# Optimization experiments

Hardware: AMD Instinct MI355X
Metric: run time of the kernel (lower is better)

The kernel has to match this reference:

```python
import jax, jax.numpy as jnp
import numpy as np

STRIDE = 1

def setup_inputs() -> dict:
    key = jax.random.key(0)
    k1, k2, k3 = jax.random.split(key, 3)
    x = jax.random.normal(k1, (32, 64, 112, 112), dtype=jnp.float32)
    weight = jax.random.normal(k2, (128, 64, 3, 3), dtype=jnp.float32)
    bias = jax.random.normal(k3, (128,), dtype=jnp.float32)
    return {"x": x, "weight": weight, "bias": bias}

def reference(x, weight, bias):
    # Naive per-patch multiply-sum conv == standard cross-correlation conv2d,
    # stride=1, no padding (VALID).  x: (N,Cin,H,W), weight: (Cout,Cin,kH,kW)
    out = jax.lax.conv_general_dilated(
        x, weight,
        window_strides=(STRIDE, STRIDE),
        padding="VALID",
        dimension_numbers=("NCHW", "OIHW", "NCHW"),
    )
    return out + bias[None, :, None, None]
```

## Files before the change

### kernel.cpp

```cpp
#include <hip/hip_runtime.h>


#define CIN   64
#define COUT  128
#define INH   112
#define INW   112
#define HW    (INH*INW)
#define OUTH  110
#define OUTW  110
#define NB    32
#define KTOT  576
#define NPIX  (NB*OUTH*OUTW)

typedef __attribute__((ext_vector_type(8))) short short8;
typedef __attribute__((ext_vector_type(4))) float f32x4;

static __device__ __forceinline__ unsigned short f2bf(float f) {
    union { float f; unsigned int u; } v; v.f = f;
    return (unsigned short)((v.u + 0x7FFF + ((v.u >> 16) & 1)) >> 16);
}

__global__ __launch_bounds__(256) void prepack_w(const float* __restrict__ w,
                                                 unsigned short* __restrict__ ap) {
    int flat = blockIdx.x * 256 + threadIdx.x;
    int m = flat / KTOT;
    int k = flat - m * KTOT;
    int khw = k >> 6, ci = k & 63;
    int kh = khw / 3, kw = khw - kh * 3;
    float v = w[((m * CIN + ci) * 3 + kh) * 3 + kw];
    ap[((k >> 3) * COUT + m) * 8 + (k & 7)] = f2bf(v);
}

__global__ __launch_bounds__(256, 2) void conv_gemm(const float* __restrict__ x,
                                                    const unsigned short* __restrict__ ap,
                                                    const float* __restrict__ bias,
                                                    float* __restrict__ out) {
    __shared__ unsigned short ldsB[32256];

    const int flat0 = blockIdx.y * 55 + blockIdx.x;
    const int flat  = (flat0 & 7) * 220 + (flat0 >> 3);
    const int n   = flat / 55;
    const int ohp = flat - n * 55;
    const int oh0 = ohp * 2;
    const int t   = threadIdx.x;

    const int lane = t & 63;
    const int wv   = t >> 6;
    const int m_base  = (wv >> 1) * 64;
    const int px_base = (wv & 1) * 128;
    const int l16  = lane & 15;
    const int quad = lane >> 4;

    const short8* A = (const short8*)ap;

    auto loadA = [&](short8* a, int kc) {
#pragma unroll
        for (int i = 0; i < 4; ++i)
            a[i] = A[(kc * 4 + quad) * COUT + (m_base + i * 16 + l16)];
    };
    auto loadBh = [&](short8* b, int kc, int h) {
        const int khw = kc >> 1;
        const int kh = khw / 3, kw = khw - kh * 3;
        const int ci0 = (kc & 1) * 32 + quad * 8;
#pragma unroll
        for (int jj = 0; jj < 4; ++jj) {
            int px = px_base + (h * 4 + jj) * 16 + l16;
            int orow = px >> 7;
            int ow = px & 127;
            ow = (ow < OUTW) ? ow : (OUTW - 1);
            b[jj] = *(const short8*)&ldsB[((orow + kh) * INW + ow + kw) * 72 + ci0];
        }
    };

    short8 a0[4], a1[4], bA[4], bB[4];
    loadA(a0, 0);

    {
        const int cq  = lane & 7;
        const int cip = wv * 8 + ((lane >> 3) & 3) + 4 * (lane >> 5);
        const float* p0 = x + ((size_t)n * CIN + 2 * cip) * HW + (size_t)oh0 * INW;
        unsigned int* ldsW = (unsigned int*)ldsB;
#pragma unroll 8
        for (int i = 0; i < 56; ++i) {
            int cell = i * 8 + cq;
            int r = cell / 112, w = cell - r * 112;
            float va = p0[r * INW + w];
            float vb = p0[HW + r * INW + w];
            ldsW[cell * 36 + cip] = (unsigned int)f2bf(va) | ((unsigned int)f2bf(vb) << 16);
        }
    }
    loadA(a1, 1);
    __syncthreads();

    f32x4 acc[4][8] = {};
    loadBh(bA, 0, 0);

#pragma unroll
    for (int kc = 0; kc < 18; kc += 2) {
        loadBh(bB, kc, 1);
        __builtin_amdgcn_s_setprio(1);
#pragma unroll
        for (int i = 0; i < 4; ++i)
#pragma unroll
            for (int jj = 0; jj < 4; ++jj)
                acc[i][jj] = __builtin_amdgcn_mfma_f32_16x16x32_bf16(a0[i], bA[jj], acc[i][jj], 0, 0, 0);
        __builtin_amdgcn_s_setprio(0);
        loadBh(bA, kc + 1, 0);
        __builtin_amdgcn_s_setprio(1);
#pragma unroll
        for (int i = 0; i < 4; ++i)
#pragma unroll
            for (int jj = 0; jj < 4; ++jj)
                acc[i][4 + jj] = __builtin_amdgcn_mfma_f32_16x16x32_bf16(a0[i], bB[jj], acc[i][4 + jj], 0, 0, 0);
        __builtin_amdgcn_s_setprio(0);
        if (kc + 2 < 18) loadA(a0, kc + 2);

        loadBh(bB, kc + 1, 1);
        __builtin_amdgcn_s_setprio(1);
#pragma unroll
        for (int i = 0; i < 4; ++i)
#pragma unroll
            for (int jj = 0; jj < 4; ++jj)
                acc[i][jj] = __builtin_amdgcn_mfma_f32_16x16x32_bf16(a1[i], bA[jj], acc[i][jj], 0, 0, 0);
        __builtin_amdgcn_s_setprio(0);
        if (kc + 2 < 18) loadBh(bA, kc + 2, 0);
        __builtin_amdgcn_s_setprio(1);
#pragma unroll
        for (int i = 0; i < 4; ++i)
#pragma unroll
            for (int jj = 0; jj < 4; ++jj)
                acc[i][4 + jj] = __builtin_amdgcn_mfma_f32_16x16x32_bf16(a1[i], bB[jj], acc[i][4 + jj], 0, 0, 0);
        __builtin_amdgcn_s_setprio(0);
        if (kc + 3 < 18) loadA(a1, kc + 3);
    }

#pragma unroll
    for (int i = 0; i < 4; ++i) {
        const int co = m_base + i * 16 + quad * 4;
#pragma unroll
        for (int j = 0; j < 8; ++j) {
            const int px = px_base + j * 16 + l16;
            const int orow = px >> 7;
            const int ow = px & 127;
            if (ow < OUTW) {
                const size_t ob = (((size_t)n * COUT + co) * OUTH + (oh0 + orow)) * OUTW + ow;
#pragma unroll
                for (int r = 0; r < 4; ++r)
                    out[ob + (size_t)r * (OUTH * OUTW)] = acc[i][j][r] + bias[co + r];
            }
        }
    }
}

#define TCO 16
__global__ __launch_bounds__(256) void conv_direct(const float* __restrict__ x,
                                                   const float* __restrict__ w,
                                                   const float* __restrict__ bias,
                                                   float* __restrict__ out) {
    int p = blockIdx.x * 256 + threadIdx.x;
    const int co0 = blockIdx.y * TCO;
    const bool valid = p < NPIX;
    if (!valid) p = 0;
    const int n = p / (OUTH * OUTW);
    const int rem = p - n * (OUTH * OUTW);
    const int oh = rem / OUTW;
    const int ow = rem - oh * OUTW;
    float acc[TCO];
#pragma unroll
    for (int t = 0; t < TCO; ++t) acc[t] = bias[co0 + t];
    const float* xb = x + ((size_t)n * CIN) * HW + (size_t)oh * INW + ow;
    const float* wb = w + (size_t)co0 * CIN * 9;
    for (int ci = 0; ci < CIN; ++ci) {
        const float* xp = xb + (size_t)ci * HW;
        const float* wp = wb + ci * 9;
#pragma unroll
        for (int kh = 0; kh < 3; ++kh) {
            const float x0 = xp[kh * INW + 0];
            const float x1 = xp[kh * INW + 1];
            const float x2 = xp[kh * INW + 2];
#pragma unroll
            for (int t = 0; t < TCO; ++t) {
                const float* wt = wp + t * (CIN * 9) + kh * 3;
                acc[t] = fmaf(x0, wt[0], acc[t]);
                acc[t] = fmaf(x1, wt[1], acc[t]);
                acc[t] = fmaf(x2, wt[2], acc[t]);
            }
        }
    }
    if (valid) {
        const size_t ob = ((size_t)n * COUT + co0) * (OUTH * OUTW) + (size_t)oh * OUTW + ow;
#pragma unroll
        for (int t = 0; t < TCO; ++t)
            out[ob + (size_t)t * (OUTH * OUTW)] = acc[t];
    }
}

extern "C" void kernel_launch(void* const* d_in, const int* in_sizes, int n_in,
                              void* d_out, int out_size, void* d_ws, size_t ws_size,
                              hipStream_t stream) {
    const float* x    = (const float*)d_in[0];
    const float* w    = (const float*)d_in[1];
    const float* bias = (const float*)d_in[2];
    float* out        = (float*)d_out;

    const size_t ap_bytes = (size_t)COUT * KTOT * 2;

    if (ws_size >= ap_bytes) {
        unsigned short* apck = (unsigned short*)d_ws;
        prepack_w<<<288, 256, 0, stream>>>(w, apck);
        conv_gemm<<<dim3(55, NB), 256, 0, stream>>>(x, apck, bias, out);
    } else {
        dim3 grid((NPIX + 255) / 256, COUT / TCO);
        conv_direct<<<grid, dim3(256), 0, stream>>>(x, w, bias, out);
    }
}
```

Measured before the change: 324.9 us.

## Split input staging by row and overlap second half with kh=0 MFMAs

Input staging into LDS is split into two halves. Rows 0-1 are loaded first, the kh=0 taps (kc 0-5) are computed, and only then are rows 2-3 staged behind a second barrier before the remaining taps run. Staging loads are also widened to float2 with a simpler per-row index calculation. The aim is to shorten the initial global-load stall before any MFMA work starts and to let later row loads overlap with compute. The cost is an extra __syncthreads and more duplicated unrolled loop code.

```diff
diff --git a/kernel.cpp b/kernel.cpp
--- a/kernel.cpp
+++ b/kernel.cpp
@@ -72,23 +72,29 @@
         }
     };
 
+    const int cq  = lane & 7;
+    const int cip = wv * 8 + ((lane >> 3) & 3) + 4 * (lane >> 5);
+    const float* xrow0 = x + ((size_t)n * CIN + 2 * cip) * HW + (size_t)oh0 * INW;
+    unsigned int* ldsW = (unsigned int*)ldsB;
+
+    auto stageRow = [&](int r) {
+        const float* p = xrow0 + (size_t)r * INW;
+        unsigned int* dst = ldsW + r * (112 * 36) + cip;
+#pragma unroll
+        for (int i = 0; i < 7; ++i) {
+            int w0 = 16 * i + 2 * cq;
+            float2 va = *(const float2*)(p + w0);
+            float2 vb = *(const float2*)(p + HW + w0);
+            dst[(w0)     * 36] = (unsigned int)f2bf(va.x) | ((unsigned int)f2bf(vb.x) << 16);
+            dst[(w0 + 1) * 36] = (unsigned int)f2bf(va.y) | ((unsigned int)f2bf(vb.y) << 16);
+        }
+    };
+
     short8 a0[4], a1[4], bA[4], bB[4];
     loadA(a0, 0);
 
-    {
-        const int cq  = lane & 7;
-        const int cip = wv * 8 + ((lane >> 3) & 3) + 4 * (lane >> 5);
-        const float* p0 = x + ((size_t)n * CIN + 2 * cip) * HW + (size_t)oh0 * INW;
-        unsigned int* ldsW = (unsigned int*)ldsB;
-#pragma unroll 8
-        for (int i = 0; i < 56; ++i) {
-            int cell = i * 8 + cq;
-            int r = cell / 112, w = cell - r * 112;
-            float va = p0[r * INW + w];
-            float vb = p0[HW + r * INW + w];
-            ldsW[cell * 36 + cip] = (unsigned int)f2bf(va) | ((unsigned int)f2bf(vb) << 16);
-        }
-    }
+    stageRow(0);
+    stageRow(1);
     loadA(a1, 1);
     __syncthreads();
 
@@ -96,7 +102,7 @@
     loadBh(bA, 0, 0);
 
 #pragma unroll
-    for (int kc = 0; kc < 18; kc += 2) {
+    for (int kc = 0; kc < 6; kc += 2) {
         loadBh(bB, kc, 1);
         __builtin_amdgcn_s_setprio(1);
 #pragma unroll
@@ -113,8 +119,51 @@
             for (int jj = 0; jj < 4; ++jj)
                 acc[i][4 + jj] = __builtin_amdgcn_mfma_f32_16x16x32_bf16(a0[i], bB[jj], acc[i][4 + jj], 0, 0, 0);
         __builtin_amdgcn_s_setprio(0);
+        loadA(a0, kc + 2);
+        loadBh(bB, kc + 1, 1);
+        __builtin_amdgcn_s_setprio(1);
+#pragma unroll
+        for (int i = 0; i < 4; ++i)
+#pragma unroll
+            for (int jj = 0; jj < 4; ++jj)
+                acc[i][jj] = __builtin_amdgcn_mfma_f32_16x16x32_bf16(a1[i], bA[jj], acc[i][jj], 0, 0, 0);
+        __builtin_amdgcn_s_setprio(0);
+        if (kc + 2 < 6) loadBh(bA, kc + 2, 0);
+        __builtin_amdgcn_s_setprio(1);
+#pragma unroll
+        for (int i = 0; i < 4; ++i)
+#pragma unroll
+            for (int jj = 0; jj < 4; ++jj)
+                acc[i][4 + jj] = __builtin_amdgcn_mfma_f32_16x16x32_bf16(a1[i], bB[jj], acc[i][4 + jj], 0, 0, 0);
+        __builtin_amdgcn_s_setprio(0);
+        loadA(a1, kc + 3);
+    }
+
+    stageRow(2);
+    stageRow(3);
+    __syncthreads();
+
+    loadBh(bA, 6, 0);
+
+#pragma unroll
+    for (int kc = 6; kc < 18; kc += 2) {
+        loadBh(bB, kc, 1);
+        __builtin_amdgcn_s_setprio(1);
+#pragma unroll
+        for (int i = 0; i < 4; ++i)
+#pragma unroll
+            for (int jj = 0; jj < 4; ++jj)
+                acc[i][jj] = __builtin_amdgcn_mfma_f32_16x16x32_bf16(a0[i], bA[jj], acc[i][jj], 0, 0, 0);
+        __builtin_amdgcn_s_setprio(0);
+        loadBh(bA, kc + 1, 0);
+        __builtin_amdgcn_s_setprio(1);
+#pragma unroll
+        for (int i = 0; i < 4; ++i)
+#pragma unroll
+            for (int jj = 0; jj < 4; ++jj)
+                acc[i][4 + jj] = __builtin_amdgcn_mfma_f32_16x16x32_bf16(a0[i], bB[jj], acc[i][4 + jj], 0, 0, 0);
+        __builtin_amdgcn_s_setprio(0);
         if (kc + 2 < 18) loadA(a0, kc + 2);
-
         loadBh(bB, kc + 1, 1);
         __builtin_amdgcn_s_setprio(1);
 #pragma unroll
```

New measurement: 325.0 us. Within noise of the previous version (+0.0%).

## Pack output pixels densely to cut padded MFMA work per wave

Applied to the files above, without the earlier changes.

Each wave pair now covers 220 output pixels as 2x112, using 7 16-pixel fragments per wave instead of 8 fragments over a 128-wide padded row. This removes roughly an eighth of the MFMA and LDS read work that was spent on padding columns. The K loop is restructured to alternate even and odd K chunks with full 7-fragment B tiles, with loads of the next chunk interleaved between MFMA groups. The B register footprint grows from 8 to 14 short8 per stage, which adds register pressure against the 2-blocks-per-SM launch bound, and the tail lanes beyond 220 pixels still compute clamped duplicates.

```diff
diff --git a/kernel.cpp b/kernel.cpp
--- a/kernel.cpp
+++ b/kernel.cpp
@@ -11,6 +11,7 @@
 #define NB    32
 #define KTOT  576
 #define NPIX  (NB*OUTH*OUTW)
+#define NFR   7
 
 typedef __attribute__((ext_vector_type(8))) short short8;
 typedef __attribute__((ext_vector_type(4))) float f32x4;
@@ -47,7 +48,7 @@
     const int lane = t & 63;
     const int wv   = t >> 6;
     const int m_base  = (wv >> 1) * 64;
-    const int px_base = (wv & 1) * 128;
+    const int px_base = (wv & 1) * 112;
     const int l16  = lane & 15;
     const int quad = lane >> 4;
 
@@ -58,22 +59,22 @@
         for (int i = 0; i < 4; ++i)
             a[i] = A[(kc * 4 + quad) * COUT + (m_base + i * 16 + l16)];
     };
-    auto loadBh = [&](short8* b, int kc, int h) {
+    auto loadB = [&](short8* b, int kc) {
         const int khw = kc >> 1;
         const int kh = khw / 3, kw = khw - kh * 3;
         const int ci0 = (kc & 1) * 32 + quad * 8;
 #pragma unroll
-        for (int jj = 0; jj < 4; ++jj) {
-            int px = px_base + (h * 4 + jj) * 16 + l16;
-            int orow = px >> 7;
-            int ow = px & 127;
+        for (int j = 0; j < NFR; ++j) {
+            int px = px_base + j * 16 + l16;
+            int orow = (px >= OUTW) ? 1 : 0;
+            int ow = px - OUTW * orow;
             ow = (ow < OUTW) ? ow : (OUTW - 1);
-            b[jj] = *(const short8*)&ldsB[((orow + kh) * INW + ow + kw) * 72 + ci0];
+            b[j] = *(const short8*)&ldsB[((orow + kh) * INW + ow + kw) * 72 + ci0];
         }
     };
 
-    short8 a0[4], a1[4], bA[4], bB[4];
-    loadA(a0, 0);
+    short8 aE[4], aO[4], bE[NFR], bO[NFR];
+    loadA(aE, 0);
 
     {
         const int cq  = lane & 7;
@@ -89,60 +90,42 @@
             ldsW[cell * 36 + cip] = (unsigned int)f2bf(va) | ((unsigned int)f2bf(vb) << 16);
         }
     }
-    loadA(a1, 1);
+    loadA(aO, 1);
     __syncthreads();
 
-    f32x4 acc[4][8] = {};
-    loadBh(bA, 0, 0);
+    f32x4 acc[4][NFR] = {};
+    loadB(bE, 0);
 
 #pragma unroll
     for (int kc = 0; kc < 18; kc += 2) {
-        loadBh(bB, kc, 1);
+        loadB(bO, kc + 1);
         __builtin_amdgcn_s_setprio(1);
 #pragma unroll
         for (int i = 0; i < 4; ++i)
 #pragma unroll
-            for (int jj = 0; jj < 4; ++jj)
-                acc[i][jj] = __builtin_amdgcn_mfma_f32_16x16x32_bf16(a0[i], bA[jj], acc[i][jj], 0, 0, 0);
+            for (int j = 0; j < NFR; ++j)
+                acc[i][j] = __builtin_amdgcn_mfma_f32_16x16x32_bf16(aE[i], bE[j], acc[i][j], 0, 0, 0);
         __builtin_amdgcn_s_setprio(0);
-        loadBh(bA, kc + 1, 0);
+        if (kc + 2 < 18) { loadA(aE, kc + 2); loadB(bE, kc + 2); }
         __builtin_amdgcn_s_setprio(1);
 #pragma unroll
         for (int i = 0; i < 4; ++i)
 #pragma unroll
-            for (int jj = 0; jj < 4; ++jj)
-                acc[i][4 + jj] = __builtin_amdgcn_mfma_f32_16x16x32_bf16(a0[i], bB[jj], acc[i][4 + jj], 0, 0, 0);
+            for (int j = 0; j < NFR; ++j)
+                acc[i][j] = __builtin_amdgcn_mfma_f32_16x16x32_bf16(aO[i], bO[j], acc[i][j], 0, 0, 0);
         __builtin_amdgcn_s_setprio(0);
-        if (kc + 2 < 18) loadA(a0, kc + 2);
-
-        loadBh(bB, kc + 1, 1);
-        __builtin_amdgcn_s_setprio(1);
-#pragma unroll
-        for (int i = 0; i < 4; ++i)
-#pragma unroll
-            for (int jj = 0; jj < 4; ++jj)
-                acc[i][jj] = __builtin_amdgcn_mfma_f32_16x16x32_bf16(a1[i], bA[jj], acc[i][jj], 0, 0, 0);
-        __builtin_amdgcn_s_setprio(0);
-        if (kc + 2 < 18) loadBh(bA, kc + 2, 0);
-        __builtin_amdgcn_s_setprio(1);
-#pragma unroll
-        for (int i = 0; i < 4; ++i)
-#pragma unroll
-            for (int jj = 0; jj < 4; ++jj)
-                acc[i][4 + jj] = __builtin_amdgcn_mfma_f32_16x16x32_bf16(a1[i], bB[jj], acc[i][4 + jj], 0, 0, 0);
-        __builtin_amdgcn_s_setprio(0);
-        if (kc + 3 < 18) loadA(a1, kc + 3);
+        if (kc + 3 < 18) loadA(aO, kc + 3);
     }
 
 #pragma unroll
     for (int i = 0; i < 4; ++i) {
         const int co = m_base + i * 16 + quad * 4;
 #pragma unroll
-        for (int j = 0; j < 8; ++j) {
+        for (int j = 0; j < NFR; ++j) {
             const int px = px_base + j * 16 + l16;
-            const int orow = px >> 7;
-            const int ow = px & 127;
-            if (ow < OUTW) {
+            const int orow = (px >= OUTW) ? 1 : 0;
+            const int ow = px - OUTW * orow;
+            if (px < 2 * OUTW) {
                 const size_t ob = (((size_t)n * COUT + co) * OUTH + (oh0 + orow)) * OUTW + ow;
 #pragma unroll
                 for (int r = 0; r < 4; ++r)
```

Measured after the change: 326.8 us. No clear change (+0.6%).
